# Optimization experiments

Measured on AMD Instinct MI355X. Metric: run time of the kernel, lower is better.

## Reference

```python
import jax, jax.numpy as jnp
import numpy as np

B, S, D = 4, 2048, 1024  # batch, seq_len, input_dim (= dk = dv)


def setup_inputs() -> dict:
    key = jax.random.key(0)
    kx, kq, kk, kv = jax.random.split(key, 4)
    scale = 1.0 / np.sqrt(D)
    return {
        "x": jax.random.normal(kx, (B, S, D), dtype=jnp.float32),
        "Wq": jax.random.normal(kq, (D, D), dtype=jnp.float32) * scale,
        "Wk": jax.random.normal(kk, (D, D), dtype=jnp.float32) * scale,
        "Wv": jax.random.normal(kv, (D, D), dtype=jnp.float32) * scale,
    }


def reference(x, Wq, Wk, Wv):
    # Linear projections (bias=False). W is [in, out].
    Q = jnp.einsum("bsd,de->bse", x, Wq)
    K = jnp.einsum("bsd,de->bse", x, Wk)
    V = jnp.einsum("bsd,de->bse", x, Wv)
    dk = Q.shape[-1]
    # scores: [B, S, S]
    scores = jnp.einsum("bqe,bke->bqk", Q, K) / jnp.sqrt(jnp.float32(dk))
    # causal mask: upper triangle (j > i) masked to -inf
    S_len = x.shape[1]
    causal = jnp.triu(jnp.ones((S_len, S_len), dtype=bool), k=1)
    scores = jnp.where(causal[None, :, :], -jnp.inf, scores)
    attn = jax.nn.softmax(scores, axis=-1)
    # dropout p=0.0 (eval): identity
    return jnp.einsum("bqk,bke->bqe", attn, V)
```

## Files before the change

kernel.cpp:

```cpp
#include <hip/hip_runtime.h>

#define S_LEN 2048
#define DMODEL 1024
#define NBATCH 4

typedef unsigned short u16;
typedef __bf16 bf16x8 __attribute__((ext_vector_type(8)));
typedef float f32x4 __attribute__((ext_vector_type(4)));

typedef __attribute__((address_space(3))) unsigned lds_u32;
typedef const __attribute__((address_space(1))) unsigned glb_u32;

__device__ __forceinline__ u16 f2bf(float f) {
  union { float f; unsigned u; } v;
  v.f = f;
  unsigned r = v.u + 0x7fffu + ((v.u >> 16) & 1u);
  return (u16)(r >> 16);
}

__device__ __forceinline__ float bf2f(u16 h) {
  union { unsigned u; float f; } v;
  v.u = ((unsigned)h) << 16;
  return v.f;
}

__global__ void convert_x_kernel(const float* __restrict__ x, u16* __restrict__ xb, long n) {
  long i = ((long)blockIdx.x * blockDim.x + threadIdx.x) * 4;
  long stride = (long)gridDim.x * blockDim.x * 4;
  for (; i < n; i += stride) {
    float4 v = *reinterpret_cast<const float4*>(x + i);
    ushort4 o;
    o.x = f2bf(v.x); o.y = f2bf(v.y); o.z = f2bf(v.z); o.w = f2bf(v.w);
    *reinterpret_cast<ushort4*>(xb + i) = o;
  }
}

__global__ void transpose_w_kernel(const float* __restrict__ W, u16* __restrict__ Wt) {
  __shared__ float tile[32][33];
  int tx = threadIdx.x, ty = threadIdx.y;
  int k0 = blockIdx.x * 32, n0 = blockIdx.y * 32;
#pragma unroll
  for (int i = 0; i < 32; i += 8)
    tile[ty + i][tx] = W[(long)(k0 + ty + i) * DMODEL + n0 + tx];
  __syncthreads();
#pragma unroll
  for (int i = 0; i < 32; i += 8)
    Wt[(long)(n0 + ty + i) * DMODEL + k0 + tx] = f2bf(tile[tx][ty + i]);
}

#define STG(SRCP, LD, ISB, H, T, BUFB) do { \
    const u16* _s = (SRCP) + (long)(H) * 128 * (LD) + (T) * 64; \
    char* _d = lds + (BUFB) * 65536 + ((ISB) ? 32768 : 0) + ((H) * 8 + w) * 2048; \
    __builtin_amdgcn_global_load_lds((glb_u32*)_s, (lds_u32*)_d, 16, 0, 0); \
    __builtin_amdgcn_global_load_lds((glb_u32*)(_s + 32), (lds_u32*)(_d + 1024), 16, 0, 0); \
  } while (0)

#define READ_A(QM) do { \
    _Pragma("unroll") \
    for (int _i = 0; _i < 4; ++_i) { \
      int _mp = (QM) * 8 + wm * 4 + _i; \
      af[_i][0] = *(const bf16x8*)(_Al + (_mp * 2 + 0) * 1024 + frag_off); \
      af[_i][1] = *(const bf16x8*)(_Al + (_mp * 2 + 1) * 1024 + frag_off); \
    } \
  } while (0)

#define READ_BQ(DST, QN) do { \
    _Pragma("unroll") \
    for (int _j = 0; _j < 2; ++_j) { \
      int _np = (QN) * 8 + wn * 2 + _j; \
      DST[_j][0] = *(const bf16x8*)(_Bl + (_np * 2 + 0) * 1024 + frag_off); \
      DST[_j][1] = *(const bf16x8*)(_Bl + (_np * 2 + 1) * 1024 + frag_off); \
    } \
  } while (0)

#define MFMA16(QM, QN, BREG) do { \
    _Pragma("unroll") \
    for (int _i = 0; _i < 4; ++_i) \
      _Pragma("unroll") \
      for (int _j = 0; _j < 2; ++_j) { \
        acc[QM][QN][_i][_j] = __builtin_amdgcn_mfma_f32_16x16x32_bf16(af[_i][0], BREG[_j][0], acc[QM][QN][_i][_j], 0, 0, 0); \
        acc[QM][QN][_i][_j] = __builtin_amdgcn_mfma_f32_16x16x32_bf16(af[_i][1], BREG[_j][1], acc[QM][QN][_i][_j], 0, 0, 0); \
      } \
  } while (0)

template<int CMODE, int CAUSAL>
__global__ __launch_bounds__(512, 2) void gemm256(
    const u16* __restrict__ A, const u16* __restrict__ B, void* __restrict__ Cptr,
    int lda, int ldb, int ldc, int Kdim,
    long sAz, long sBz, long sCz)
{
  int bm = blockIdx.x, bn = blockIdx.y, bz = blockIdx.z;
  if (CAUSAL == 1 && bn > bm) return;
  int Keff = Kdim;
  if (CAUSAL == 2) { int lim = (bm + 1) * 256; if (lim < Keff) Keff = lim; }
  int NT = Keff >> 6;

  const u16* Ab = A + (long)bz * sAz + (long)bm * 256 * lda;
  const u16* Bb = B + (long)bz * sBz + (long)bn * 256 * ldb;

  __shared__ char lds[131072];

  int tid = threadIdx.x;
  int lane = tid & 63, w = tid >> 6;
  int wm = w >> 2, wn = w & 3;
  int l15 = lane & 15, lhi = lane >> 4;
  int frag_off = (l15 * 64 + lhi * 16) ^ (((lane >> 3) & 1) << 5);

  int le = lane ^ ((lane >> 5) << 1);
  int lr = le >> 2;
  int kb = (le & 3) * 8;

  const u16* Asrc = Ab + (long)(w * 16 + lr) * lda + kb;
  const u16* Bsrc = Bb + (long)(w * 16 + lr) * ldb + kb;

  f32x4 acc[2][2][4][2];
#pragma unroll
  for (int a = 0; a < 2; ++a)
#pragma unroll
    for (int b = 0; b < 2; ++b)
#pragma unroll
      for (int c = 0; c < 4; ++c)
#pragma unroll
        for (int d = 0; d < 2; ++d)
          acc[a][b][c][d] = (f32x4){0.f, 0.f, 0.f, 0.f};

  STG(Asrc, lda, 0, 0, 0, 0); STG(Bsrc, ldb, 1, 0, 0, 0);
  STG(Asrc, lda, 0, 1, 0, 0); STG(Bsrc, ldb, 1, 1, 0, 0);
  STG(Asrc, lda, 0, 0, 1, 1); STG(Bsrc, ldb, 1, 0, 1, 1);
  asm volatile("s_waitcnt vmcnt(4)" ::: "memory");
  __builtin_amdgcn_s_barrier();

  for (int g = 0; g < NT; ++g) {
    int buf = g & 1;
    int t1 = g + 1; if (t1 >= NT) t1 -= NT;
    int t2 = g + 2; if (t2 >= NT) t2 -= NT;
    const char* _Al = lds + buf * 65536;
    const char* _Bl = _Al + 32768;
    bf16x8 af[4][2], b0[2][2], b1[2][2];

    READ_A(0);
    READ_BQ(b0, 0);
    STG(Asrc, lda, 0, 1, t1, buf ^ 1);
    __builtin_amdgcn_s_barrier();
    asm volatile("s_waitcnt lgkmcnt(0)" ::: "memory");
    __builtin_amdgcn_sched_barrier(0);
    __builtin_amdgcn_s_setprio(1);
    MFMA16(0, 0, b0);
    __builtin_amdgcn_s_setprio(0);
    __builtin_amdgcn_s_barrier();

    READ_BQ(b1, 1);
    STG(Bsrc, ldb, 1, 1, t1, buf ^ 1);
    __builtin_amdgcn_s_barrier();
    asm volatile("s_waitcnt lgkmcnt(0)" ::: "memory");
    __builtin_amdgcn_sched_barrier(0);
    __builtin_amdgcn_s_setprio(1);
    MFMA16(0, 1, b1);
    __builtin_amdgcn_s_setprio(0);
    __builtin_amdgcn_s_barrier();

    READ_A(1);
    STG(Asrc, lda, 0, 0, t2, buf);
    __builtin_amdgcn_s_barrier();
    asm volatile("s_waitcnt lgkmcnt(0)" ::: "memory");
    __builtin_amdgcn_sched_barrier(0);
    __builtin_amdgcn_s_setprio(1);
    MFMA16(1, 1, b1);
    __builtin_amdgcn_s_setprio(0);
    __builtin_amdgcn_s_barrier();

    STG(Bsrc, ldb, 1, 0, t2, buf);
    __builtin_amdgcn_s_barrier();
    __builtin_amdgcn_s_setprio(1);
    MFMA16(1, 0, b0);
    __builtin_amdgcn_s_setprio(0);
    asm volatile("s_waitcnt vmcnt(4)" ::: "memory");
    __builtin_amdgcn_s_barrier();
  }

  int Mbase = bm * 256, Nbase = bn * 256;
#pragma unroll
  for (int qm = 0; qm < 2; ++qm)
#pragma unroll
    for (int qn = 0; qn < 2; ++qn)
#pragma unroll
      for (int i = 0; i < 4; ++i)
#pragma unroll
        for (int j = 0; j < 2; ++j) {
          int r0 = Mbase + qm * 128 + wm * 64 + i * 16 + lhi * 4;
          int col = Nbase + qn * 128 + wn * 32 + j * 16 + l15;
          f32x4 v = acc[qm][qn][i][j];
          if constexpr (CMODE == 0) {
            float* C = (float*)Cptr + (long)bz * sCz;
#pragma unroll
            for (int r = 0; r < 4; ++r)
              C[(long)(r0 + r) * ldc + col] = v[r];
          } else if constexpr (CMODE == 1) {
            u16* C = (u16*)Cptr + (long)bz * sCz;
#pragma unroll
            for (int r = 0; r < 4; ++r)
              C[(long)(r0 + r) * ldc + col] = f2bf(v[r]);
          }
        }
}

template<int CMODE, int CAUSAL>
__global__ __launch_bounds__(512, 2) void gemm128(
    const u16* __restrict__ A, const u16* __restrict__ B, void* __restrict__ Cptr,
    int lda, int ldb, int ldc, int Kdim,
    long sAz, long sBz, long sCz)
{
  int bm = blockIdx.x, bn = blockIdx.y, bz = blockIdx.z;
  int Keff = Kdim;
  if (CAUSAL == 2) { int lim = (bm + 1) * 128; if (lim < Keff) Keff = lim; }
  int NT = Keff >> 6;

  const u16* Ab = A + (long)bz * sAz + (long)bm * 128 * lda;
  const u16* Bb = B + (long)bz * sBz + (long)bn * 256 * ldb;

  __shared__ char lds[98304];

  int tid = threadIdx.x;
  int lane = tid & 63, w = tid >> 6;
  int wm = w >> 2, wn = w & 3;
  int l15 = lane & 15, lhi = lane >> 4;
  int frag_off = (l15 * 64 + lhi * 16) ^ (((lane >> 3) & 1) << 5);

  int le = lane ^ ((lane >> 5) << 1);
  int lr = le >> 2;
  int kb = (le & 3) * 8;

  const u16* Asrc = Ab + (long)(w * 16 + lr) * lda + kb;
  const u16* Bsrc = Bb + (long)(w * 16 + lr) * ldb + kb;

#define STG_A1(T, BUFB) do { \
    const u16* _s = Asrc + (T) * 64; \
    char* _d = lds + (BUFB) * 49152 + w * 2048; \
    __builtin_amdgcn_global_load_lds((glb_u32*)_s, (lds_u32*)_d, 16, 0, 0); \
    __builtin_amdgcn_global_load_lds((glb_u32*)(_s + 32), (lds_u32*)(_d + 1024), 16, 0, 0); \
  } while (0)
#define STG_B1H0(T, BUFB) do { \
    const u16* _s = Bsrc + (T) * 64; \
    char* _d = lds + (BUFB) * 49152 + 16384 + w * 2048; \
    __builtin_amdgcn_global_load_lds((glb_u32*)_s, (lds_u32*)_d, 16, 0, 0); \
    __builtin_amdgcn_global_load_lds((glb_u32*)(_s + 32), (lds_u32*)(_d + 1024), 16, 0, 0); \
  } while (0)
#define STG_B1H1(T, BUFB) do { \
    const u16* _s = Bsrc + (long)128 * ldb + (T) * 64; \
    char* _d = lds + (BUFB) * 49152 + 16384 + (8 + w) * 2048; \
    __builtin_amdgcn_global_load_lds((glb_u32*)_s, (lds_u32*)_d, 16, 0, 0); \
    __builtin_amdgcn_global_load_lds((glb_u32*)(_s + 32), (lds_u32*)(_d + 1024), 16, 0, 0); \
  } while (0)

  f32x4 acc[4][4];
#pragma unroll
  for (int i = 0; i < 4; ++i)
#pragma unroll
    for (int j = 0; j < 4; ++j)
      acc[i][j] = (f32x4){0.f, 0.f, 0.f, 0.f};

  STG_A1(0, 0); STG_B1H0(0, 0); STG_B1H1(0, 0);
  asm volatile("s_waitcnt vmcnt(0)" ::: "memory");
  __builtin_amdgcn_s_barrier();

  for (int g = 0; g < NT; ++g) {
    int buf = g & 1;
    const char* _Al = lds + buf * 49152;
    const char* _Bl = _Al + 16384;
    bf16x8 af[4][2], bfr[2][2];

#pragma unroll
    for (int i = 0; i < 4; ++i) {
      af[i][0] = *(const bf16x8*)(_Al + ((wm * 4 + i) * 2 + 0) * 1024 + frag_off);
      af[i][1] = *(const bf16x8*)(_Al + ((wm * 4 + i) * 2 + 1) * 1024 + frag_off);
    }
#pragma unroll
    for (int j = 0; j < 2; ++j) {
      bfr[j][0] = *(const bf16x8*)(_Bl + ((wn * 4 + j) * 2 + 0) * 1024 + frag_off);
      bfr[j][1] = *(const bf16x8*)(_Bl + ((wn * 4 + j) * 2 + 1) * 1024 + frag_off);
    }
    if (g + 1 < NT) { STG_A1(g + 1, buf ^ 1); STG_B1H0(g + 1, buf ^ 1); }
    __builtin_amdgcn_s_barrier();
    asm volatile("s_waitcnt lgkmcnt(0)" ::: "memory");
    __builtin_amdgcn_sched_barrier(0);
    __builtin_amdgcn_s_setprio(1);
#pragma unroll
    for (int i = 0; i < 4; ++i)
#pragma unroll
      for (int j = 0; j < 2; ++j) {
        acc[i][j] = __builtin_amdgcn_mfma_f32_16x16x32_bf16(af[i][0], bfr[j][0], acc[i][j], 0, 0, 0);
        acc[i][j] = __builtin_amdgcn_mfma_f32_16x16x32_bf16(af[i][1], bfr[j][1], acc[i][j], 0, 0, 0);
      }
    __builtin_amdgcn_s_setprio(0);
    __builtin_amdgcn_s_barrier();

#pragma unroll
    for (int j = 0; j < 2; ++j) {
      bfr[j][0] = *(const bf16x8*)(_Bl + ((wn * 4 + 2 + j) * 2 + 0) * 1024 + frag_off);
      bfr[j][1] = *(const bf16x8*)(_Bl + ((wn * 4 + 2 + j) * 2 + 1) * 1024 + frag_off);
    }
    if (g + 1 < NT) STG_B1H1(g + 1, buf ^ 1);
    __builtin_amdgcn_s_barrier();
    asm volatile("s_waitcnt lgkmcnt(0)" ::: "memory");
    __builtin_amdgcn_sched_barrier(0);
    __builtin_amdgcn_s_setprio(1);
#pragma unroll
    for (int i = 0; i < 4; ++i)
#pragma unroll
      for (int j = 0; j < 2; ++j) {
        acc[i][2 + j] = __builtin_amdgcn_mfma_f32_16x16x32_bf16(af[i][0], bfr[j][0], acc[i][2 + j], 0, 0, 0);
        acc[i][2 + j] = __builtin_amdgcn_mfma_f32_16x16x32_bf16(af[i][1], bfr[j][1], acc[i][2 + j], 0, 0, 0);
      }
    __builtin_amdgcn_s_setprio(0);
    asm volatile("s_waitcnt vmcnt(0)" ::: "memory");
    __builtin_amdgcn_s_barrier();
  }
#undef STG_A1
#undef STG_B1H0
#undef STG_B1H1

  int Mbase = bm * 128, Nbase = bn * 256;
#pragma unroll
  for (int i = 0; i < 4; ++i)
#pragma unroll
    for (int j = 0; j < 4; ++j) {
      int r0 = Mbase + wm * 64 + i * 16 + lhi * 4;
      int col = Nbase + wn * 64 + j * 16 + l15;
      f32x4 v = acc[i][j];
      if constexpr (CMODE == 0) {
        float* C = (float*)Cptr + (long)bz * sCz;
#pragma unroll
        for (int r = 0; r < 4; ++r)
          C[(long)(r0 + r) * ldc + col] = v[r];
      } else {
        if (col < 2048) {
          u16* dst = (u16*)Cptr + (col >= 1024 ? 8388608 : 0);
          int c = col & 1023;
#pragma unroll
          for (int r = 0; r < 4; ++r)
            dst[(long)(r0 + r) * 1024 + c] = f2bf(v[r]);
        } else {
          u16* Vt = (u16*)Cptr + 16777216;
          int e = col - 2048;
          int bb = r0 >> 11, s = r0 & 2047;
          ushort4 u;
          u.x = f2bf(v[0]); u.y = f2bf(v[1]); u.z = f2bf(v[2]); u.w = f2bf(v[3]);
          *reinterpret_cast<ushort4*>(Vt + ((long)bb * 1024 + e) * 2048 + s) = u;
        }
      }
    }
}

__global__ __launch_bounds__(256) void softmax1p(const u16* __restrict__ sc,
                                                 u16* __restrict__ P) {
  int q = blockIdx.x, b = blockIdx.y;
  const u16* srow = sc + ((long)b * S_LEN + q) * S_LEN;
  u16* prow = P + ((long)b * S_LEN + q) * S_LEN;
  int n = q + 1;
  int nz = ((q >> 8) + 1) << 8;
  int tid = threadIdx.x;
  int j0 = tid * 8;
  const float scale = 0.03125f;

  __shared__ float red[8];

  float vs[8];
#pragma unroll
  for (int e = 0; e < 8; ++e) vs[e] = -1e30f;
  if (j0 < n) {
    ushort4 a = *reinterpret_cast<const ushort4*>(srow + j0);
    ushort4 c = *reinterpret_cast<const ushort4*>(srow + j0 + 4);
    vs[0] = bf2f(a.x) * scale; vs[1] = bf2f(a.y) * scale;
    vs[2] = bf2f(a.z) * scale; vs[3] = bf2f(a.w) * scale;
    vs[4] = bf2f(c.x) * scale; vs[5] = bf2f(c.y) * scale;
    vs[6] = bf2f(c.z) * scale; vs[7] = bf2f(c.w) * scale;
#pragma unroll
    for (int e = 0; e < 8; ++e)
      if (j0 + e >= n) vs[e] = -1e30f;
  }

  float m = -1e30f;
#pragma unroll
  for (int e = 0; e < 8; ++e) m = fmaxf(m, vs[e]);
#pragma unroll
  for (int off = 32; off > 0; off >>= 1) m = fmaxf(m, __shfl_xor(m, off, 64));
  if ((tid & 63) == 0) red[tid >> 6] = m;
  __syncthreads();
  float ms = fmaxf(fmaxf(red[0], red[1]), fmaxf(red[2], red[3]));

  float p[8];
  float s = 0.f;
#pragma unroll
  for (int e = 0; e < 8; ++e) { p[e] = __expf(vs[e] - ms); s += (j0 + e < n) ? p[e] : 0.f; }
#pragma unroll
  for (int off = 32; off > 0; off >>= 1) s += __shfl_xor(s, off, 64);
  __syncthreads();
  if ((tid & 63) == 0) red[4 + (tid >> 6)] = s;
  __syncthreads();
  float inv = 1.f / (red[4] + red[5] + red[6] + red[7]);

  if (j0 < nz) {
    ushort4 o0, o1;
    o0.x = (j0 + 0 < n) ? f2bf(p[0] * inv) : (u16)0;
    o0.y = (j0 + 1 < n) ? f2bf(p[1] * inv) : (u16)0;
    o0.z = (j0 + 2 < n) ? f2bf(p[2] * inv) : (u16)0;
    o0.w = (j0 + 3 < n) ? f2bf(p[3] * inv) : (u16)0;
    o1.x = (j0 + 4 < n) ? f2bf(p[4] * inv) : (u16)0;
    o1.y = (j0 + 5 < n) ? f2bf(p[5] * inv) : (u16)0;
    o1.z = (j0 + 6 < n) ? f2bf(p[6] * inv) : (u16)0;
    o1.w = (j0 + 7 < n) ? f2bf(p[7] * inv) : (u16)0;
    *reinterpret_cast<ushort4*>(prow + j0) = o0;
    *reinterpret_cast<ushort4*>(prow + j0 + 4) = o1;
  }
}

extern "C" void kernel_launch(void* const* d_in, const int* in_sizes, int n_in,
                              void* d_out, int out_size, void* d_ws, size_t ws_size,
                              hipStream_t stream) {
  const float* x  = (const float*)d_in[0];
  const float* Wq = (const float*)d_in[1];
  const float* Wk = (const float*)d_in[2];
  const float* Wv = (const float*)d_in[3];
  float* out = (float*)d_out;

  char* ws = (char*)d_ws;
  u16* xb  = (u16*)(ws);
  u16* wtb = (u16*)(ws + 16777216);
  u16* Qb  = (u16*)(ws + 23068672);
  u16* Kb  = (u16*)(ws + 39845888);
  u16* Vtb = (u16*)(ws + 56623104);
  u16* scb = (u16*)(ws + 73400320);
  u16* P   = (u16*)(ws + 106954752);

  long nx = (long)NBATCH * S_LEN * DMODEL;
  convert_x_kernel<<<2048, 256, 0, stream>>>(x, xb, nx);

  dim3 tb(32, 8);
  transpose_w_kernel<<<dim3(32, 32), tb, 0, stream>>>(Wq, wtb);
  transpose_w_kernel<<<dim3(32, 32), tb, 0, stream>>>(Wk, wtb + 1024 * 1024);
  transpose_w_kernel<<<dim3(32, 32), tb, 0, stream>>>(Wv, wtb + 2 * 1024 * 1024);

  gemm128<3, 0><<<dim3(64, 12, 1), 512, 0, stream>>>(
      xb, wtb, Qb, DMODEL, DMODEL, 0, DMODEL, 0, 0, 0);

  gemm256<1, 1><<<dim3(8, 8, 4), 512, 0, stream>>>(
      Qb, Kb, scb, DMODEL, DMODEL, S_LEN, DMODEL,
      (long)S_LEN * DMODEL, (long)S_LEN * DMODEL, (long)S_LEN * S_LEN);

  softmax1p<<<dim3(S_LEN, NBATCH), 256, 0, stream>>>(scb, P);

  gemm128<0, 2><<<dim3(16, 4, 4), 512, 0, stream>>>(
      P, Vtb, out, S_LEN, S_LEN, DMODEL, S_LEN,
      (long)S_LEN * S_LEN, (long)DMODEL * S_LEN, (long)S_LEN * DMODEL);
}
```

Measured before the change: 170.7 us.

## Split-K the causal PV GEMM into 512-wide chunks with a bf16 partial reduction

The causal P·V GEMM now splits the K dimension into chunks of 512, so the grid grows from 256 to up to 1024 blocks and rows with little work no longer sit beside rows with a lot. Each chunk writes a bf16 partial tile into workspace that reuses the scores buffer, and a new reduce kernel sums the partials into the fp32 output. This is meant to fix load imbalance and low occupancy from the triangular K extent. In exchange it adds an extra kernel launch, extra global traffic for the partials, and precision loss from rounding the partials to bf16.

```diff
diff --git a/kernel.cpp b/kernel.cpp
--- a/kernel.cpp
+++ b/kernel.cpp
@@ -92,7 +92,6 @@
   int bm = blockIdx.x, bn = blockIdx.y, bz = blockIdx.z;
   if (CAUSAL == 1 && bn > bm) return;
   int Keff = Kdim;
-  if (CAUSAL == 2) { int lim = (bm + 1) * 256; if (lim < Keff) Keff = lim; }
   int NT = Keff >> 6;
 
   const u16* Ab = A + (long)bz * sAz + (long)bm * 256 * lda;
@@ -211,12 +210,24 @@
     long sAz, long sBz, long sCz)
 {
   int bm = blockIdx.x, bn = blockIdx.y, bz = blockIdx.z;
+  int k0 = 0;
   int Keff = Kdim;
-  if (CAUSAL == 2) { int lim = (bm + 1) * 128; if (lim < Keff) Keff = lim; }
+  int slot = 0;
+  if constexpr (CAUSAL == 3) {
+    int c = bz & 3;
+    bz = bz >> 2;
+    int Klim = (bm + 1) * 128;
+    k0 = c * 512;
+    if (k0 >= Klim) return;
+    int k1 = k0 + 512; if (k1 > Klim) k1 = Klim;
+    Keff = k1 - k0;
+    int q = bm >> 2, s = bm & 3;
+    slot = bz * 40 + (q + 1) * (2 * q + s) + c;
+  }
   int NT = Keff >> 6;
 
-  const u16* Ab = A + (long)bz * sAz + (long)bm * 128 * lda;
-  const u16* Bb = B + (long)bz * sBz + (long)bn * 256 * ldb;
+  const u16* Ab = A + (long)bz * sAz + (long)bm * 128 * lda + k0;
+  const u16* Bb = B + (long)bz * sBz + (long)bn * 256 * ldb + k0;
 
   __shared__ char lds[98304];
 
@@ -332,6 +343,12 @@
 #pragma unroll
         for (int r = 0; r < 4; ++r)
           C[(long)(r0 + r) * ldc + col] = v[r];
+      } else if constexpr (CMODE == 4) {
+        u16* Pp = (u16*)Cptr + (long)slot * 131072;
+        int rl = wm * 64 + i * 16 + lhi * 4;
+#pragma unroll
+        for (int r = 0; r < 4; ++r)
+          Pp[(long)(rl + r) * 1024 + col] = f2bf(v[r]);
       } else {
         if (col < 2048) {
           u16* dst = (u16*)Cptr + (col >= 1024 ? 8388608 : 0);
@@ -414,6 +431,28 @@
   }
 }
 
+__global__ __launch_bounds__(256) void reduce_pv(const u16* __restrict__ partial,
+                                                 float* __restrict__ out) {
+  long i4 = (long)blockIdx.x * 256 + threadIdx.x;
+  int e4 = (int)(i4 & 255);
+  long t = i4 >> 8;
+  int rr = (int)(t & 2047);
+  int b = (int)(t >> 11);
+  int bm = rr >> 7, r128 = rr & 127;
+  int q = bm >> 2, s = bm & 3;
+  int off = (q + 1) * (2 * q + s);
+  int cnt = q + 1;
+
+  const u16* base = partial + ((long)(b * 40 + off)) * 131072 + (long)r128 * 1024 + e4 * 4;
+  float a0 = 0.f, a1 = 0.f, a2 = 0.f, a3 = 0.f;
+  for (int c = 0; c < cnt; ++c) {
+    ushort4 vv = *reinterpret_cast<const ushort4*>(base + (long)c * 131072);
+    a0 += bf2f(vv.x); a1 += bf2f(vv.y); a2 += bf2f(vv.z); a3 += bf2f(vv.w);
+  }
+  float4 o = make_float4(a0, a1, a2, a3);
+  *reinterpret_cast<float4*>(out + ((long)b * 2048 + rr) * 1024 + e4 * 4) = o;
+}
+
 extern "C" void kernel_launch(void* const* d_in, const int* in_sizes, int n_in,
                               void* d_out, int out_size, void* d_ws, size_t ws_size,
                               hipStream_t stream) {
@@ -424,13 +463,14 @@
   float* out = (float*)d_out;
 
   char* ws = (char*)d_ws;
-  u16* xb  = (u16*)(ws);
-  u16* wtb = (u16*)(ws + 16777216);
-  u16* Qb  = (u16*)(ws + 23068672);
-  u16* Kb  = (u16*)(ws + 39845888);
-  u16* Vtb = (u16*)(ws + 56623104);
-  u16* scb = (u16*)(ws + 73400320);
-  u16* P   = (u16*)(ws + 106954752);
+  u16* xb   = (u16*)(ws);
+  u16* wtb  = (u16*)(ws + 16777216);
+  u16* Qb   = (u16*)(ws + 23068672);
+  u16* Kb   = (u16*)(ws + 39845888);
+  u16* Vtb  = (u16*)(ws + 56623104);
+  u16* scb  = (u16*)(ws + 73400320);
+  u16* part = (u16*)(ws + 73400320);
+  u16* P    = (u16*)(ws + 115343360);
 
   long nx = (long)NBATCH * S_LEN * DMODEL;
   convert_x_kernel<<<2048, 256, 0, stream>>>(x, xb, nx);
@@ -449,7 +489,9 @@
 
   softmax1p<<<dim3(S_LEN, NBATCH), 256, 0, stream>>>(scb, P);
 
-  gemm128<0, 2><<<dim3(16, 4, 4), 512, 0, stream>>>(
-      P, Vtb, out, S_LEN, S_LEN, DMODEL, S_LEN,
-      (long)S_LEN * S_LEN, (long)DMODEL * S_LEN, (long)S_LEN * DMODEL);
-}
+  gemm128<4, 3><<<dim3(16, 4, 16), 512, 0, stream>>>(
+      P, Vtb, part, S_LEN, S_LEN, 0, S_LEN,
+      (long)S_LEN * S_LEN, (long)DMODEL * S_LEN, 0);
+
+  reduce_pv<<<8192, 256, 0, stream>>>(part, out);
+}
```

New measurement: 190.3 us. 11.5% more time.
